# Kernel optimization log

Measured on AMD Instinct MI355X. Metric: run time of the kernel, lower is better.

## Reference

```python
import jax, jax.numpy as jnp
import numpy as np

S, D, H, HD, CQ, CKV, O = 2048, 2048, 16, 128, 96, 512, 2048


def _linear_params(k, fan_in, fan_out):
    kw, kb = jax.random.split(k)
    lim = 1.0 / np.sqrt(fan_in)
    w = jax.random.uniform(kw, (fan_out, fan_in), minval=-lim, maxval=lim, dtype=jnp.float32)
    b = jax.random.uniform(kb, (fan_out,), minval=-lim, maxval=lim, dtype=jnp.float32)
    return w, b


def setup_inputs() -> dict:
    key = jax.random.key(0)
    ks = jax.random.split(key, 8)
    x = jax.random.normal(ks[0], (S, D), dtype=jnp.float32)
    # standard RoPE tables: theta_i = 10000^(-2i/hd), rotate-half layout
    pos = jnp.arange(S, dtype=jnp.float32)[:, None]              # (S, 1)
    inv_freq = 1.0 / (10000.0 ** (jnp.arange(0, HD, 2, dtype=jnp.float32) / HD))  # (HD/2,)
    ang = pos * inv_freq[None, :]                                 # (S, HD/2)
    rope_cos = jnp.concatenate([jnp.cos(ang), jnp.cos(ang)], axis=-1)  # (S, HD)
    rope_sin = jnp.concatenate([jnp.sin(ang), jnp.sin(ang)], axis=-1)  # (S, HD)
    wq_down, bq_down = _linear_params(ks[1], D, CQ)
    wq_up, bq_up = _linear_params(ks[2], CQ, H * HD)
    wkv_down, bkv_down = _linear_params(ks[3], D, CKV)
    wk_up, bk_up = _linear_params(ks[4], CKV, H * HD)
    wv_up, bv_up = _linear_params(ks[5], CKV, H * HD)
    wo, bo = _linear_params(ks[6], H * HD, O)
    return dict(x=x, rope_cos=rope_cos, rope_sin=rope_sin,
                wq_down=wq_down, bq_down=bq_down, wq_up=wq_up, bq_up=bq_up,
                wkv_down=wkv_down, bkv_down=bkv_down, wk_up=wk_up, bk_up=bk_up,
                wv_up=wv_up, bv_up=bv_up, wo=wo, bo=bo)


def _rope(xh, cos, sin):
    # xh: (S, H, hd); cos/sin: (S, hd) broadcast over heads
    half = xh.shape[-1] // 2
    x1, x2 = xh[..., :half], xh[..., half:]
    rot = jnp.concatenate([-x2, x1], axis=-1)
    return xh * cos[:, None, :] + rot * sin[:, None, :]


def reference(x, rope_cos, rope_sin, wq_down, bq_down, wq_up, bq_up,
              wkv_down, bkv_down, wk_up, bk_up, wv_up, bv_up, wo, bo):
    s = x.shape[0]
    # low-rank Q path: down then up (compressed_q_size < head_dim branch)
    c_q = x @ wq_down.T + bq_down                                  # (S, CQ)
    q = (c_q @ wq_up.T + bq_up).reshape(s, H, HD)                  # (S, H, hd)
    q = _rope(q, rope_cos, rope_sin)
    # shared compressed KV path
    c_kv = x @ wkv_down.T + bkv_down                               # (S, CKV)
    k = _rope((c_kv @ wk_up.T + bk_up).reshape(s, H, HD), rope_cos, rope_sin)
    v = (c_kv @ wv_up.T + bv_up).reshape(s, H, HD)
    # scaled dot-product attention per head (softmax in fp32 as in source)
    q = q / jnp.sqrt(jnp.asarray(HD, q.dtype))
    logits = jnp.einsum('shd,Shd->hsS', q, k)                      # (H, S, S)
    weights = jax.nn.softmax(logits.astype(jnp.float32), axis=-1).astype(logits.dtype)
    attn = jnp.einsum('hsS,Shd->shd', weights, v).reshape(s, H * HD)
    return attn @ wo.T + bo                                        # (S, O)
```

## Files before the change

kernel.cpp:

```cpp
#include <hip/hip_runtime.h>
#include <cstdint>
#include <cstddef>

typedef unsigned short u16;
typedef float f32x4 __attribute__((ext_vector_type(4)));
typedef short s16x8 __attribute__((ext_vector_type(8)));

#define DI __device__ __forceinline__

static constexpr int S_  = 2048;
static constexpr int D_  = 2048;
static constexpr int H_  = 16;
static constexpr int HD_ = 128;
static constexpr int HHD = 2048;
static constexpr int CQP = 128;
static constexpr int NCAT = 640;
static constexpr int CKV_ = 512;
static constexpr float QSCALE = 0.12751743360294163f;

DI u16 f2bf(float f) {
  unsigned u = __float_as_uint(f);
  u += 0x7fffu + ((u >> 16) & 1u);
  return (u16)(u >> 16);
}
DI float bf2f(u16 h) { return __uint_as_float(((unsigned)h) << 16); }

DI void store_c(float* C, long long i, float v) { C[i] = v; }
DI void store_c(u16* C, long long i, float v) { C[i] = f2bf(v); }

template <int CTRL>
DI float dppf(float x) {
  return __uint_as_float((unsigned)__builtin_amdgcn_mov_dpp(
      (int)__float_as_uint(x), CTRL, 0xf, 0xf, true));
}
DI float red_max16(float x) {
  x = fmaxf(x, dppf<0xB1>(x));
  x = fmaxf(x, dppf<0x4E>(x));
  x = fmaxf(x, dppf<0x141>(x));
  x = fmaxf(x, dppf<0x140>(x));
  return x;
}
DI float red_sum16(float x) {
  x += dppf<0xB1>(x);
  x += dppf<0x4E>(x);
  x += dppf<0x141>(x);
  x += dppf<0x140>(x);
  return x;
}

#define GLD16(g, l)                                                        \
  __builtin_amdgcn_global_load_lds(                                        \
      (__attribute__((address_space(1))) void*)(void*)(const void*)(g),    \
      (__attribute__((address_space(3))) void*)(l), 16, 0, 0)

template <typename OutT, int BCOL, int BROW, int BN>
DI void gemm_core(u16* __restrict__ Asm, u16* __restrict__ Bsm,
                  const u16* __restrict__ A, const u16* __restrict__ B,
                  OutT* __restrict__ C,
                  const float* __restrict__ bias_col,
                  const float* __restrict__ bias_row,
                  int K, int lda, int ldb, int ldc) {
  constexpr int MI = (BN == 128) ? 4 : 2;
  constexpr int NI = 4;
  constexpr int NCH = 8 + BN / 16;
  constexpr int NC4 = NCH / 4;
  const int tid  = threadIdx.x;
  const int w    = tid >> 6;
  const int lane = tid & 63;
  const int lr   = lane & 15;
  const int lq   = lane >> 4;
  const long long m0 = (long long)blockIdx.y * 128;
  const long long n0 = (long long)blockIdx.x * BN;
  const int wr = (BN == 128) ? (w >> 1) * 64 : w * 32;
  const int wc = (BN == 128) ? (w & 1) * 64 : 0;

  f32x4 acc[MI][NI];
#pragma unroll
  for (int i = 0; i < MI; ++i)
#pragma unroll
    for (int j = 0; j < NI; ++j)
#pragma unroll
      for (int r = 0; r < 4; ++r) acc[i][j][r] = 0.f;

  const int rch = lane >> 2, cch = (lane & 3) * 8;
  const u16* gsrc[NC4];
  u16* ldst[NC4];
  int bstep[NC4];
#pragma unroll
  for (int ci = 0; ci < NC4; ++ci) {
    const int c = w + ci * 4;
    if (c < 8) {
      gsrc[ci] = A + (m0 + c * 16 + rch) * lda + cch;
      ldst[ci] = &Asm[c * 512];
      bstep[ci] = 128 * 32;
    } else {
      gsrc[ci] = B + (n0 + (c - 8) * 16 + rch) * ldb + cch;
      ldst[ci] = &Bsm[(c - 8) * 512];
      bstep[ci] = BN * 32;
    }
  }
  auto stage = [&](int kt, int b) {
#pragma unroll
    for (int ci = 0; ci < NC4; ++ci) GLD16(gsrc[ci] + kt, ldst[ci] + b * bstep[ci]);
  };

  stage(0, 0);
  int cur = 0;
  for (int kt = 0; kt < K; kt += 32) {
    __syncthreads();
    if (kt + 32 < K) stage(kt + 32, cur ^ 1);
    const u16* Ab = &Asm[cur * 128 * 32];
    const u16* Bb = &Bsm[cur * BN * 32];

    s16x8 af[MI], bfr[NI];
#pragma unroll
    for (int tm = 0; tm < MI; ++tm)
      af[tm] = *(const s16x8*)&Ab[(wr + tm * 16 + lr) * 32 + lq * 8];
#pragma unroll
    for (int tn = 0; tn < NI; ++tn)
      bfr[tn] = *(const s16x8*)&Bb[(wc + tn * 16 + lr) * 32 + lq * 8];
#pragma unroll
    for (int tm = 0; tm < MI; ++tm)
#pragma unroll
      for (int tn = 0; tn < NI; ++tn)
        acc[tm][tn] = __builtin_amdgcn_mfma_f32_16x16x32_bf16(af[tm], bfr[tn],
                                                              acc[tm][tn], 0, 0, 0);
    cur ^= 1;
  }

#pragma unroll
  for (int tm = 0; tm < MI; ++tm)
#pragma unroll
    for (int tn = 0; tn < NI; ++tn) {
      const long long col = n0 + wc + tn * 16 + lr;
      float bc = BCOL ? bias_col[col] : 0.f;
#pragma unroll
      for (int r = 0; r < 4; ++r) {
        const long long row = m0 + wr + tm * 16 + lq * 4 + r;
        float v = acc[tm][tn][r] + bc;
        if (BROW) v += bias_row[row];
        store_c(C, row * (long long)ldc + col, v);
      }
    }
}

template <typename OutT, int BCOL, int BROW, int BN>
__global__ __launch_bounds__(256) void gemm_bt(
    const u16* __restrict__ A, const u16* __restrict__ B, OutT* __restrict__ C,
    const float* __restrict__ bias_col, const float* __restrict__ bias_row,
    int K, int lda, int ldb, int ldc,
    long long sA, long long sB, long long sC) {
  __shared__ __align__(16) u16 As[2 * 128 * 32];
  __shared__ __align__(16) u16 Bs[2 * BN * 32];
  gemm_core<OutT, BCOL, BROW, BN>(
      As, Bs, A + (long long)blockIdx.z * sA, B + (long long)blockIdx.z * sB,
      C + (long long)blockIdx.z * sC, bias_col, bias_row, K, lda, ldb, ldc);
}

__global__ __launch_bounds__(256, 3) void up3(
    const u16* __restrict__ ccat, const u16* __restrict__ wqu,
    const u16* __restrict__ wku, const u16* __restrict__ wvu,
    const float* __restrict__ bq_up, const float* __restrict__ bk_up,
    const float* __restrict__ bv_up,
    u16* __restrict__ qb, u16* __restrict__ kb, u16* __restrict__ vT) {
  __shared__ __align__(16) u16 As[2 * 128 * 32];
  __shared__ __align__(16) u16 Bs[2 * 128 * 32];
  if (blockIdx.z == 0)
    gemm_core<u16, 1, 0, 128>(As, Bs, ccat, wqu, qb, bq_up, nullptr,
                              CQP, NCAT, CQP, HHD);
  else if (blockIdx.z == 1)
    gemm_core<u16, 1, 0, 128>(As, Bs, ccat + CQP, wku, kb, bk_up, nullptr,
                              CKV_, NCAT, CKV_, HHD);
  else
    gemm_core<u16, 0, 1, 128>(As, Bs, wvu, ccat + CQP, vT, nullptr, bv_up,
                              CKV_, CKV_, NCAT, S_);
}

DI void store4(float* d, long long e, float4 s) { *(float4*)(d + e) = s; }
DI void store4(u16* d, long long e, float4 s) {
  unsigned lo = (unsigned)f2bf(s.x) | ((unsigned)f2bf(s.y) << 16);
  unsigned hi = (unsigned)f2bf(s.z) | ((unsigned)f2bf(s.w) << 16);
  *(uint2*)(d + e) = make_uint2(lo, hi);
}
template <typename OutT>
__global__ __launch_bounds__(256) void combine_z(
    const float* __restrict__ p, long long zs, int nz,
    const float* __restrict__ bias, OutT* __restrict__ dst, int ldc, int n4) {
  int i = blockIdx.x * 256 + threadIdx.x;
  if (i >= n4) return;
  long long e = (long long)i * 4;
  float4 s = *(const float4*)(p + e);
  for (int z = 1; z < nz; ++z) {
    float4 t = *(const float4*)(p + (long long)z * zs + e);
    s.x += t.x; s.y += t.y; s.z += t.z; s.w += t.w;
  }
  int c = (int)(e % ldc);
  s.x += bias[c]; s.y += bias[c + 1]; s.z += bias[c + 2]; s.w += bias[c + 3];
  store4(dst, e, s);
}

__global__ __launch_bounds__(256, 2) void flash_attn(
    const u16* __restrict__ Q, const u16* __restrict__ Kg,
    const u16* __restrict__ Vt, u16* __restrict__ Og) {
  __shared__ __align__(16) u16 Ks[128 * 128];
  __shared__ __align__(16) u16 Vs[128 * 128];
  __shared__ __align__(16) u16 Ps[64 * 128];
  const int h = blockIdx.x;
  const int t = blockIdx.y;
  const int tid = threadIdx.x;
  const int w = tid >> 6, lane = tid & 63, lr = lane & 15, lq = lane >> 4;
  const int g = w >> 1;
  const int wq = w & 1;
  const int qw = t * 64 + wq * 32;
  const int tr = tid >> 4;
  const int csw = (tid & 15) ^ (tr & 7);

  s16x8 qf[2][4];
#pragma unroll
  for (int mi = 0; mi < 2; ++mi)
#pragma unroll
    for (int kst = 0; kst < 4; ++kst)
      qf[mi][kst] = *(const s16x8*)&Q[(size_t)(qw + mi * 16 + lr) * HHD +
                                      h * HD_ + kst * 32 + lq * 8];

  f32x4 oacc[2][8];
  float m[2][4], l[2][4];
#pragma unroll
  for (int mi = 0; mi < 2; ++mi) {
#pragma unroll
    for (int r = 0; r < 4; ++r) { m[mi][r] = -1.0e38f; l[mi][r] = 0.f; }
#pragma unroll
    for (int f = 0; f < 8; ++f)
#pragma unroll
      for (int r = 0; r < 4; ++r) oacc[mi][f][r] = 0.f;
  }

  auto stage_k = [&](int j) {
    const u16* s0 = Kg + (size_t)(j * 128 + tr) * HHD + h * HD_ + csw * 8;
#pragma unroll
    for (int i = 0; i < 8; ++i)
      GLD16(s0 + (size_t)i * 16 * HHD, &Ks[i * 2048 + w * 512]);
  };
  auto stage_v = [&](int j) {
    const u16* s0 = Vt + (size_t)(h * HD_ + tr) * S_ + j * 128 + csw * 8;
#pragma unroll
    for (int i = 0; i < 8; ++i)
      GLD16(s0 + (size_t)i * 16 * S_, &Vs[i * 2048 + w * 512]);
  };

  stage_k(0);
  stage_v(0);
  __syncthreads();

  for (int j = 0; j < 16; ++j) {
    f32x4 sacc[2][4];
#pragma unroll
    for (int mi = 0; mi < 2; ++mi)
#pragma unroll
      for (int f = 0; f < 4; ++f)
#pragma unroll
        for (int r = 0; r < 4; ++r) sacc[mi][f][r] = 0.f;
#pragma unroll
    for (int kst = 0; kst < 4; ++kst)
#pragma unroll
      for (int f = 0; f < 4; ++f) {
        const int key = g * 64 + f * 16 + lr;
        s16x8 kf = *(const s16x8*)
            &Ks[key * 128 + (((kst * 4 + lq) ^ (key & 7)) << 3)];
        sacc[0][f] = __builtin_amdgcn_mfma_f32_16x16x32_bf16(qf[0][kst], kf,
                                                             sacc[0][f], 0, 0, 0);
        sacc[1][f] = __builtin_amdgcn_mfma_f32_16x16x32_bf16(qf[1][kst], kf,
                                                             sacc[1][f], 0, 0, 0);
      }

#pragma unroll
    for (int mi = 0; mi < 2; ++mi)
#pragma unroll
      for (int r = 0; r < 4; ++r) {
        float mx = sacc[mi][0][r];
#pragma unroll
        for (int f = 1; f < 4; ++f) mx = fmaxf(mx, sacc[mi][f][r]);
        mx = red_max16(mx);
        float mn = fmaxf(m[mi][r], mx);
        float al = exp2f(m[mi][r] - mn);
        m[mi][r] = mn;
        float sum = 0.f;
#pragma unroll
        for (int f = 0; f < 4; ++f) {
          float p = exp2f(sacc[mi][f][r] - mn);
          sacc[mi][f][r] = p;
          sum += p;
        }
        sum = red_sum16(sum);
        l[mi][r] = l[mi][r] * al + sum;
#pragma unroll
        for (int f = 0; f < 8; ++f) oacc[mi][f][r] *= al;
      }

#pragma unroll
    for (int mi = 0; mi < 2; ++mi)
#pragma unroll
      for (int r = 0; r < 4; ++r) {
        const int q = wq * 32 + mi * 16 + lq * 4 + r;
#pragma unroll
        for (int f = 0; f < 4; ++f) {
          const int ch = (g * 8 + f * 2 + (lr >> 3)) ^ (q & 7);
          Ps[q * 128 + ch * 8 + (lr & 7)] = f2bf(sacc[mi][f][r]);
        }
      }

    __syncthreads();
    if (j < 15) stage_k(j + 1);

#pragma unroll
    for (int kst = 0; kst < 2; ++kst) {
      const int chA = (g * 8 + kst * 4 + lq) ^ (lr & 7);
      s16x8 pa0 = *(const s16x8*)&Ps[(wq * 32 + lr) * 128 + chA * 8];
      s16x8 pa1 = *(const s16x8*)&Ps[(wq * 32 + 16 + lr) * 128 + chA * 8];
#pragma unroll
      for (int f = 0; f < 8; ++f) {
        const int d = f * 16 + lr;
        s16x8 vf = *(const s16x8*)
            &Vs[d * 128 + (((g * 8 + kst * 4 + lq) ^ (d & 7)) << 3)];
        oacc[0][f] = __builtin_amdgcn_mfma_f32_16x16x32_bf16(pa0, vf,
                                                             oacc[0][f], 0, 0, 0);
        oacc[1][f] = __builtin_amdgcn_mfma_f32_16x16x32_bf16(pa1, vf,
                                                             oacc[1][f], 0, 0, 0);
      }
    }

    __syncthreads();
    if (j < 15) stage_v(j + 1);
  }

  float* KsF = (float*)Ks;
  float* mlF = (float*)Ps;
  if (g == 1) {
#pragma unroll
    for (int mi = 0; mi < 2; ++mi)
#pragma unroll
      for (int r = 0; r < 4; ++r) {
        const int q = wq * 32 + mi * 16 + lq * 4 + r;
        if (lr == 0) { mlF[q * 2] = m[mi][r]; mlF[q * 2 + 1] = l[mi][r]; }
#pragma unroll
        for (int f = 0; f < 8; ++f)
          KsF[q * 128 + f * 16 + lr] = oacc[mi][f][r];
      }
  }
  __syncthreads();
  if (g == 0) {
#pragma unroll
    for (int mi = 0; mi < 2; ++mi)
#pragma unroll
      for (int r = 0; r < 4; ++r) {
        const int q = wq * 32 + mi * 16 + lq * 4 + r;
        float m1 = mlF[q * 2], l1 = mlF[q * 2 + 1];
        float M = fmaxf(m[mi][r], m1);
        float w0 = exp2f(m[mi][r] - M), w1 = exp2f(m1 - M);
        float inv = 1.f / (w0 * l[mi][r] + w1 * l1);
        w0 *= inv; w1 *= inv;
#pragma unroll
        for (int f = 0; f < 8; ++f) {
          float o = w0 * oacc[mi][f][r] + w1 * KsF[q * 128 + f * 16 + lr];
          Og[(size_t)(t * 64 + q) * HHD + h * HD_ + f * 16 + lr] = f2bf(o);
        }
      }
  }
}

DI void cast4(const float* __restrict__ s, u16* __restrict__ d, int v) {
  float4 f = ((const float4*)s)[v];
  unsigned lo = (unsigned)f2bf(f.x) | ((unsigned)f2bf(f.y) << 16);
  unsigned hi = (unsigned)f2bf(f.z) | ((unsigned)f2bf(f.w) << 16);
  ((uint2*)d)[v] = make_uint2(lo, hi);
}
DI void store_bf4(u16* __restrict__ d, long long i, float4 f) {
  unsigned lo = (unsigned)f2bf(f.x) | ((unsigned)f2bf(f.y) << 16);
  unsigned hi = (unsigned)f2bf(f.z) | ((unsigned)f2bf(f.w) << 16);
  *(uint2*)(d + i) = make_uint2(lo, hi);
}
static constexpr int PV_XB   = 1048576;
static constexpr int PV_WCAT = 327680;
static constexpr int PV_WQU  = 65536;
static constexpr int PV_WKU  = 262144;
static constexpr int PV_WVU  = 262144;
static constexpr int PV_WOB  = 1048576;
static constexpr int PV_BCAT = 160;
static constexpr int PV_TOT  = PV_XB + PV_WCAT + PV_WQU + PV_WKU + PV_WVU + PV_WOB + PV_BCAT;

__global__ __launch_bounds__(256) void prep(
    const float* __restrict__ x, const float* __restrict__ wqd_s,
    const float* __restrict__ wkvd_s, const float* __restrict__ wqu_s,
    const float* __restrict__ wku_s, const float* __restrict__ wvu_s,
    const float* __restrict__ wo_s, const float* __restrict__ bqd_s,
    const float* __restrict__ bkvd_s,
    u16* __restrict__ xb, u16* __restrict__ wcat, u16* __restrict__ wqu,
    u16* __restrict__ wku, u16* __restrict__ wvu, u16* __restrict__ wob,
    float* __restrict__ bcat) {
  int v = blockIdx.x * 256 + threadIdx.x;
  if (v >= PV_TOT) return;
  if (v < PV_XB) { cast4(x, xb, v); return; }
  v -= PV_XB;
  if (v < PV_WCAT) {
    int i = v * 4, n = i >> 11, k = i & 2047;
    float4 o = make_float4(0.f, 0.f, 0.f, 0.f);
    if (n < 96)        o = *(const float4*)&wqd_s[n * D_ + k];
    else if (n >= 128) o = *(const float4*)&wkvd_s[(n - 128) * D_ + k];
    store_bf4(wcat, i, o);
    return;
  }
  v -= PV_WCAT;
  if (v < PV_WQU) {
    int i = v * 4, r = i >> 7, c = i & 127;
    float4 o = (c < 96) ? *(const float4*)&wqu_s[r * 96 + c]
                        : make_float4(0.f, 0.f, 0.f, 0.f);
    store_bf4(wqu, i, o);
    return;
  }
  v -= PV_WQU;
  if (v < PV_WKU) { cast4(wku_s, wku, v); return; }
  v -= PV_WKU;
  if (v < PV_WVU) { cast4(wvu_s, wvu, v); return; }
  v -= PV_WVU;
  if (v < PV_WOB) { cast4(wo_s, wob, v); return; }
  v -= PV_WOB;
  {
    int i = v * 4;
    float4 o;
    float* po = &o.x;
#pragma unroll
    for (int jj = 0; jj < 4; ++jj) {
      int e = i + jj;
      po[jj] = (e < 96) ? bqd_s[e] : (e < 128 ? 0.f : bkvd_s[e - 128]);
    }
    *(float4*)&bcat[i] = o;
  }
}

__global__ __launch_bounds__(256) void rope2(u16* __restrict__ qb,
                                             u16* __restrict__ kb,
                                             const float* __restrict__ cs,
                                             const float* __restrict__ sn) {
  int id = blockIdx.x * 256 + threadIdx.x;
  const bool isq = id < S_ * H_ * 64;
  if (!isq) id -= S_ * H_ * 64;
  u16* X = isq ? qb : kb;
  const float scale = isq ? QSCALE : 1.0f;
  int d = id & 63;
  int h = (id >> 6) & 15;
  int s = id >> 10;
  long long b = (long long)s * HHD + h * HD_ + d;
  float x1 = bf2f(X[b]), x2 = bf2f(X[b + 64]);
  int cb = s * HD_ + d;
  float o1 = (x1 * cs[cb] - x2 * sn[cb]) * scale;
  float o2 = (x2 * cs[cb + 64] + x1 * sn[cb + 64]) * scale;
  X[b] = f2bf(o1);
  X[b + 64] = f2bf(o2);
}

extern "C" void kernel_launch(void* const* d_in, const int* in_sizes, int n_in,
                              void* d_out, int out_size, void* d_ws, size_t ws_size,
                              hipStream_t stream) {
  (void)in_sizes; (void)n_in; (void)out_size; (void)ws_size;
  const float* x        = (const float*)d_in[0];
  const float* rc       = (const float*)d_in[1];
  const float* rs       = (const float*)d_in[2];
  const float* wq_down  = (const float*)d_in[3];
  const float* bq_down  = (const float*)d_in[4];
  const float* wq_up    = (const float*)d_in[5];
  const float* bq_up    = (const float*)d_in[6];
  const float* wkv_down = (const float*)d_in[7];
  const float* bkv_down = (const float*)d_in[8];
  const float* wk_up    = (const float*)d_in[9];
  const float* bk_up    = (const float*)d_in[10];
  const float* wv_up    = (const float*)d_in[11];
  const float* bv_up    = (const float*)d_in[12];
  const float* wo       = (const float*)d_in[13];
  const float* bo       = (const float*)d_in[14];
  float* out = (float*)d_out;

  char* ws = (char*)d_ws;
  size_t off = 0;
  auto alloc = [&](size_t bytes) -> void* {
    off = (off + 255) & ~(size_t)255;
    void* p = ws + off;
    off += bytes;
    return p;
  };

  u16* xb      = (u16*)alloc((size_t)S_ * D_ * 2);
  u16* wcat    = (u16*)alloc((size_t)NCAT * D_ * 2);
  float* bcat  = (float*)alloc(NCAT * 4);
  u16* wqu     = (u16*)alloc((size_t)HHD * CQP * 2);
  u16* wku     = (u16*)alloc((size_t)HHD * CKV_ * 2);
  u16* wvu     = (u16*)alloc((size_t)HHD * CKV_ * 2);
  u16* wob     = (u16*)alloc((size_t)D_ * HHD * 2);
  u16* ccat    = (u16*)alloc((size_t)S_ * NCAT * 2);
  u16* qb      = (u16*)alloc((size_t)S_ * HHD * 2);
  u16* kb      = (u16*)alloc((size_t)S_ * HHD * 2);
  u16* vT      = (u16*)alloc((size_t)HHD * S_ * 2);
  u16* attnb   = (u16*)alloc((size_t)S_ * HHD * 2);
  float* pool  = (float*)alloc((size_t)2 * S_ * D_ * 4);
  float* pcat  = pool;
  float* pout  = pool;

  prep<<<(PV_TOT + 255) / 256, 256, 0, stream>>>(
      x, wq_down, wkv_down, wq_up, wk_up, wv_up, wo, bq_down, bkv_down,
      xb, wcat, wqu, wku, wvu, wob, bcat);

  gemm_bt<float, 0, 0, 64><<<dim3(NCAT / 64, 16, 4), 256, 0, stream>>>(
      xb, wcat, pcat, nullptr, nullptr, 512, D_, D_, NCAT,
      512, 512, (long long)S_ * NCAT);
  combine_z<u16><<<(S_ * NCAT / 4 + 255) / 256, 256, 0, stream>>>(
      pcat, (long long)S_ * NCAT, 4, bcat, ccat, NCAT, S_ * NCAT / 4);

  up3<<<dim3(16, 16, 3), 256, 0, stream>>>(
      ccat, wqu, wku, wvu, bq_up, bk_up, bv_up, qb, kb, vT);

  rope2<<<(2 * S_ * H_ * 64) / 256, 256, 0, stream>>>(qb, kb, rc, rs);

  flash_attn<<<dim3(H_, S_ / 64, 1), 256, 0, stream>>>(qb, kb, vT, attnb);

  gemm_bt<float, 0, 0, 128><<<dim3(16, 16, 2), 256, 0, stream>>>(
      attnb, wob, pout, nullptr, nullptr, 1024, HHD, HHD, D_,
      1024, 1024, (long long)S_ * D_);
  combine_z<float><<<(S_ * D_ / 4 + 255) / 256, 256, 0, stream>>>(
      pout, (long long)S_ * D_, 2, bo, out, D_, S_ * D_ / 4);
}
```

Measured before the change: 272.4 us.

## Fuse RoPE into up-projection epilogue and skip redundant softmax rescaling

Removes the separate rope2 kernel and applies RoPE plus the query scale inside the up-projection GEMM epilogue. The B-fragment column mapping is changed so each wave holds both halves (d and d+64) of a head. In flash attention, the running max rescale of the accumulators is skipped when no row max grows, and the row-sum reduction across lanes is deferred to the end. This saves a full read-modify-write pass over Q and K and some per-tile exp and shuffle work. The cost is a more complex epilogue with extra cos/sin loads.

```diff
diff --git a/kernel.cpp b/kernel.cpp
--- a/kernel.cpp
+++ b/kernel.cpp
@@ -53,13 +53,15 @@
       (__attribute__((address_space(1))) void*)(void*)(const void*)(g),    \
       (__attribute__((address_space(3))) void*)(l), 16, 0, 0)
 
-template <typename OutT, int BCOL, int BROW, int BN>
+template <typename OutT, int BCOL, int BROW, int ROPE, int BN>
 DI void gemm_core(u16* __restrict__ Asm, u16* __restrict__ Bsm,
                   const u16* __restrict__ A, const u16* __restrict__ B,
                   OutT* __restrict__ C,
                   const float* __restrict__ bias_col,
                   const float* __restrict__ bias_row,
-                  int K, int lda, int ldb, int ldc) {
+                  int K, int lda, int ldb, int ldc,
+                  const float* __restrict__ rcs, const float* __restrict__ rsn,
+                  float scale) {
   constexpr int MI = (BN == 128) ? 4 : 2;
   constexpr int NI = 4;
   constexpr int NCH = 8 + BN / 16;
@@ -117,8 +119,11 @@
     for (int tm = 0; tm < MI; ++tm)
       af[tm] = *(const s16x8*)&Ab[(wr + tm * 16 + lr) * 32 + lq * 8];
 #pragma unroll
-    for (int tn = 0; tn < NI; ++tn)
-      bfr[tn] = *(const s16x8*)&Bb[(wc + tn * 16 + lr) * 32 + lq * 8];
+    for (int tn = 0; tn < NI; ++tn) {
+      const int cb = ROPE ? ((w & 1) * 32 + (tn & 1) * 16 + (tn >> 1) * 64)
+                          : (wc + tn * 16);
+      bfr[tn] = *(const s16x8*)&Bb[(cb + lr) * 32 + lq * 8];
+    }
 #pragma unroll
     for (int tm = 0; tm < MI; ++tm)
 #pragma unroll
@@ -128,20 +133,43 @@
     cur ^= 1;
   }
 
-#pragma unroll
-  for (int tm = 0; tm < MI; ++tm)
-#pragma unroll
-    for (int tn = 0; tn < NI; ++tn) {
-      const long long col = n0 + wc + tn * 16 + lr;
-      float bc = BCOL ? bias_col[col] : 0.f;
-#pragma unroll
-      for (int r = 0; r < 4; ++r) {
-        const long long row = m0 + wr + tm * 16 + lq * 4 + r;
-        float v = acc[tm][tn][r] + bc;
-        if (BROW) v += bias_row[row];
-        store_c(C, row * (long long)ldc + col, v);
-      }
-    }
+  if (ROPE) {
+#pragma unroll
+    for (int tm = 0; tm < MI; ++tm)
+#pragma unroll
+      for (int tn = 0; tn < 2; ++tn) {
+        const long long col1 = n0 + (w & 1) * 32 + tn * 16 + lr;
+        const long long col2 = col1 + 64;
+        const float bc1 = bias_col[col1];
+        const float bc2 = bias_col[col2];
+        const int dd = (int)(col1 & 127);
+#pragma unroll
+        for (int r = 0; r < 4; ++r) {
+          const long long row = m0 + wr + tm * 16 + lq * 4 + r;
+          const float c = rcs[row * 128 + dd];
+          const float s = rsn[row * 128 + dd];
+          const float v1 = acc[tm][tn][r] + bc1;
+          const float v2 = acc[tm][tn + 2][r] + bc2;
+          store_c(C, row * (long long)ldc + col1, (v1 * c - v2 * s) * scale);
+          store_c(C, row * (long long)ldc + col2, (v2 * c + v1 * s) * scale);
+        }
+      }
+  } else {
+#pragma unroll
+    for (int tm = 0; tm < MI; ++tm)
+#pragma unroll
+      for (int tn = 0; tn < NI; ++tn) {
+        const long long col = n0 + wc + tn * 16 + lr;
+        float bc = BCOL ? bias_col[col] : 0.f;
+#pragma unroll
+        for (int r = 0; r < 4; ++r) {
+          const long long row = m0 + wr + tm * 16 + lq * 4 + r;
+          float v = acc[tm][tn][r] + bc;
+          if (BROW) v += bias_row[row];
+          store_c(C, row * (long long)ldc + col, v);
+        }
+      }
+  }
 }
 
 template <typename OutT, int BCOL, int BROW, int BN>
@@ -152,9 +180,10 @@
     long long sA, long long sB, long long sC) {
   __shared__ __align__(16) u16 As[2 * 128 * 32];
   __shared__ __align__(16) u16 Bs[2 * BN * 32];
-  gemm_core<OutT, BCOL, BROW, BN>(
+  gemm_core<OutT, BCOL, BROW, 0, BN>(
       As, Bs, A + (long long)blockIdx.z * sA, B + (long long)blockIdx.z * sB,
-      C + (long long)blockIdx.z * sC, bias_col, bias_row, K, lda, ldb, ldc);
+      C + (long long)blockIdx.z * sC, bias_col, bias_row, K, lda, ldb, ldc,
+      nullptr, nullptr, 0.f);
 }
 
 __global__ __launch_bounds__(256, 3) void up3(
@@ -162,18 +191,19 @@
     const u16* __restrict__ wku, const u16* __restrict__ wvu,
     const float* __restrict__ bq_up, const float* __restrict__ bk_up,
     const float* __restrict__ bv_up,
+    const float* __restrict__ rcs, const float* __restrict__ rsn,
     u16* __restrict__ qb, u16* __restrict__ kb, u16* __restrict__ vT) {
   __shared__ __align__(16) u16 As[2 * 128 * 32];
   __shared__ __align__(16) u16 Bs[2 * 128 * 32];
   if (blockIdx.z == 0)
-    gemm_core<u16, 1, 0, 128>(As, Bs, ccat, wqu, qb, bq_up, nullptr,
-                              CQP, NCAT, CQP, HHD);
+    gemm_core<u16, 1, 0, 1, 128>(As, Bs, ccat, wqu, qb, bq_up, nullptr,
+                                 CQP, NCAT, CQP, HHD, rcs, rsn, QSCALE);
   else if (blockIdx.z == 1)
-    gemm_core<u16, 1, 0, 128>(As, Bs, ccat + CQP, wku, kb, bk_up, nullptr,
-                              CKV_, NCAT, CKV_, HHD);
+    gemm_core<u16, 1, 0, 1, 128>(As, Bs, ccat + CQP, wku, kb, bk_up, nullptr,
+                                 CKV_, NCAT, CKV_, HHD, rcs, rsn, 1.0f);
   else
-    gemm_core<u16, 0, 1, 128>(As, Bs, wvu, ccat + CQP, vT, nullptr, bv_up,
-                              CKV_, CKV_, NCAT, S_);
+    gemm_core<u16, 0, 1, 0, 128>(As, Bs, wvu, ccat + CQP, vT, nullptr, bv_up,
+                                 CKV_, CKV_, NCAT, S_, nullptr, nullptr, 0.f);
 }
 
 DI void store4(float* d, long long e, float4 s) { *(float4*)(d + e) = s; }
@@ -274,28 +304,40 @@
       }
 
 #pragma unroll
-    for (int mi = 0; mi < 2; ++mi)
+    for (int mi = 0; mi < 2; ++mi) {
+      float mx[4];
+      bool need = false;
 #pragma unroll
       for (int r = 0; r < 4; ++r) {
-        float mx = sacc[mi][0][r];
-#pragma unroll
-        for (int f = 1; f < 4; ++f) mx = fmaxf(mx, sacc[mi][f][r]);
-        mx = red_max16(mx);
-        float mn = fmaxf(m[mi][r], mx);
-        float al = exp2f(m[mi][r] - mn);
-        m[mi][r] = mn;
+        float v = sacc[mi][0][r];
+#pragma unroll
+        for (int f = 1; f < 4; ++f) v = fmaxf(v, sacc[mi][f][r]);
+        mx[r] = red_max16(v);
+        need = need || (mx[r] > m[mi][r]);
+      }
+      if (__any(need)) {
+#pragma unroll
+        for (int r = 0; r < 4; ++r) {
+          float mn = fmaxf(m[mi][r], mx[r]);
+          float al = exp2f(m[mi][r] - mn);
+          m[mi][r] = mn;
+          l[mi][r] *= al;
+#pragma unroll
+          for (int f = 0; f < 8; ++f) oacc[mi][f][r] *= al;
+        }
+      }
+#pragma unroll
+      for (int r = 0; r < 4; ++r) {
         float sum = 0.f;
 #pragma unroll
         for (int f = 0; f < 4; ++f) {
-          float p = exp2f(sacc[mi][f][r] - mn);
+          float p = exp2f(sacc[mi][f][r] - m[mi][r]);
           sacc[mi][f][r] = p;
           sum += p;
         }
-        sum = red_sum16(sum);
-        l[mi][r] = l[mi][r] * al + sum;
-#pragma unroll
-        for (int f = 0; f < 8; ++f) oacc[mi][f][r] *= al;
-      }
+        l[mi][r] += sum;
+      }
+    }
 
 #pragma unroll
     for (int mi = 0; mi < 2; ++mi)
@@ -333,6 +375,12 @@
     if (j < 15) stage_v(j + 1);
   }
 
+  float lf[2][4];
+#pragma unroll
+  for (int mi = 0; mi < 2; ++mi)
+#pragma unroll
+    for (int r = 0; r < 4; ++r) lf[mi][r] = red_sum16(l[mi][r]);
+
   float* KsF = (float*)Ks;
   float* mlF = (float*)Ps;
   if (g == 1) {
@@ -341,7 +389,7 @@
 #pragma unroll
       for (int r = 0; r < 4; ++r) {
         const int q = wq * 32 + mi * 16 + lq * 4 + r;
-        if (lr == 0) { mlF[q * 2] = m[mi][r]; mlF[q * 2 + 1] = l[mi][r]; }
+        if (lr == 0) { mlF[q * 2] = m[mi][r]; mlF[q * 2 + 1] = lf[mi][r]; }
 #pragma unroll
         for (int f = 0; f < 8; ++f)
           KsF[q * 128 + f * 16 + lr] = oacc[mi][f][r];
@@ -357,7 +405,7 @@
         float m1 = mlF[q * 2], l1 = mlF[q * 2 + 1];
         float M = fmaxf(m[mi][r], m1);
         float w0 = exp2f(m[mi][r] - M), w1 = exp2f(m1 - M);
-        float inv = 1.f / (w0 * l[mi][r] + w1 * l1);
+        float inv = 1.f / (w0 * lf[mi][r] + w1 * l1);
         w0 *= inv; w1 *= inv;
 #pragma unroll
         for (int f = 0; f < 8; ++f) {
@@ -437,27 +485,6 @@
   }
 }
 
-__global__ __launch_bounds__(256) void rope2(u16* __restrict__ qb,
-                                             u16* __restrict__ kb,
-                                             const float* __restrict__ cs,
-                                             const float* __restrict__ sn) {
-  int id = blockIdx.x * 256 + threadIdx.x;
-  const bool isq = id < S_ * H_ * 64;
-  if (!isq) id -= S_ * H_ * 64;
-  u16* X = isq ? qb : kb;
-  const float scale = isq ? QSCALE : 1.0f;
-  int d = id & 63;
-  int h = (id >> 6) & 15;
-  int s = id >> 10;
-  long long b = (long long)s * HHD + h * HD_ + d;
-  float x1 = bf2f(X[b]), x2 = bf2f(X[b + 64]);
-  int cb = s * HD_ + d;
-  float o1 = (x1 * cs[cb] - x2 * sn[cb]) * scale;
-  float o2 = (x2 * cs[cb + 64] + x1 * sn[cb + 64]) * scale;
-  X[b] = f2bf(o1);
-  X[b + 64] = f2bf(o2);
-}
-
 extern "C" void kernel_launch(void* const* d_in, const int* in_sizes, int n_in,
                               void* d_out, int out_size, void* d_ws, size_t ws_size,
                               hipStream_t stream) {
@@ -515,9 +542,7 @@
       pcat, (long long)S_ * NCAT, 4, bcat, ccat, NCAT, S_ * NCAT / 4);
 
   up3<<<dim3(16, 16, 3), 256, 0, stream>>>(
-      ccat, wqu, wku, wvu, bq_up, bk_up, bv_up, qb, kb, vT);
-
-  rope2<<<(2 * S_ * H_ * 64) / 256, 256, 0, stream>>>(qb, kb, rc, rs);
+      ccat, wqu, wku, wvu, bq_up, bk_up, bv_up, rc, rs, qb, kb, vT);
 
   flash_attn<<<dim3(H_, S_ / 64, 1), 256, 0, stream>>>(qb, kb, vT, attnb);
 
```

New measurement: 268.5 us. Within noise of the previous version (-1.4%).
